# Performance work log

Hardware: AMD Instinct MI355X
Metric: run time of the kernel (lower is better)

Reference implementation:

```python
import jax, jax.numpy as jnp
import numpy as np


def setup_inputs() -> dict:
    key = jax.random.key(0)
    k1, k2, k3, k4, k5 = jax.random.split(key, 5)
    B, S, D, F, E = 4, 4096, 1024, 2048, 8
    top_k = 2
    num_tokens = B * S
    capacity = max(int(num_tokens / E * 1.25), 4)  # 2560
    scale = 0.02
    return {
        "x": jax.random.normal(k1, (B, S, D), dtype=jnp.float32),
        "gate_w": jax.random.normal(k2, (D, E), dtype=jnp.float32) * scale,
        "w_gate": jax.random.normal(k3, (E, D, F), dtype=jnp.float32) * scale,
        "w_up": jax.random.normal(k4, (E, D, F), dtype=jnp.float32) * scale,
        "w_down": jax.random.normal(k5, (E, F, D), dtype=jnp.float32) * scale,
        "num_experts": E,
        "top_k": top_k,
        "capacity": capacity,
    }


AUX_LOSS_WEIGHT = 0.01


def reference(x, gate_w, w_gate, w_up, w_down, num_experts, top_k, capacity):
    B, S, D = x.shape
    N = B * S
    x_flat = x.reshape(N, D)

    # ---- Router ----
    logits = x_flat @ gate_w                      # [N, E]
    probs = jax.nn.softmax(logits, axis=-1)
    weights, indices = jax.lax.top_k(probs, top_k)  # [N, K]
    weights = weights / jnp.sum(weights, axis=-1, keepdims=True)

    # ---- Capacity-based dispatch ----
    indices_flat = indices.reshape(-1)            # [N*K]
    x_rep = jnp.repeat(x_flat, top_k, axis=0)     # [N*K, D]
    expert_mask = jax.nn.one_hot(indices_flat, num_experts, dtype=jnp.int32)  # [N*K, E]
    token_priority = jnp.cumsum(expert_mask, axis=0) * expert_mask
    token_rank = jnp.sum(token_priority, axis=1)  # [N*K], 1-based rank within expert
    valid = (token_rank > 0) & (token_rank <= capacity)
    gather_idx = indices_flat * capacity + (token_rank - 1)  # [N*K]

    total_slots = num_experts * capacity
    # drop-mode scatter: invalid rows are sent out-of-bounds and dropped
    safe_idx = jnp.where(valid, gather_idx, total_slots)
    dispatched = jnp.zeros((total_slots, D), dtype=x.dtype)
    dispatched = dispatched.at[safe_idx].set(x_rep, mode="drop")
    dispatched = dispatched.reshape(num_experts, capacity, D)  # [E, C, D]

    # ---- Fused experts (grouped BMM, SwiGLU) ----
    gate = jnp.einsum("ecd,edf->ecf", dispatched, w_gate)
    up = jnp.einsum("ecd,edf->ecf", dispatched, w_up)
    hidden = jax.nn.silu(gate) * up
    expert_out = jnp.einsum("ecf,efd->ecd", hidden, w_down)
    expert_out_flat = expert_out.reshape(total_slots, D)

    # ---- Combine (row-aligned gather; dropped tokens contribute zero) ----
    gathered = expert_out_flat[jnp.clip(gather_idx, 0, total_slots - 1)]
    combined = jnp.where(valid[:, None], gathered, jnp.zeros((), dtype=x.dtype))
    combined = combined.reshape(N, top_k, D)
    output = jnp.sum(combined * weights[:, :, None], axis=1)  # [N, D]

    # ---- Aux load-balance loss ----
    mask = jax.nn.one_hot(indices, num_experts, dtype=jnp.float32).sum(axis=1)  # [N, E]
    f = mask.sum(axis=0) / (N * top_k + 1e-9)
    P = probs.mean(axis=0)
    aux_loss = num_experts * jnp.sum(f * P) * AUX_LOSS_WEIGHT

    return output.reshape(B, S, D), aux_loss
```

## Files before the change

### kernel.cpp

```cpp
#include <hip/hip_runtime.h>
#include <stdint.h>

#define N_TOK 16384
#define DIM   1024
#define NEXP  8
#define FF    2048
#define CAP   2560
#define NSLOT (NEXP*CAP)

using f32x4  = __attribute__((ext_vector_type(4))) float;
using bf16x8 = __attribute__((ext_vector_type(8))) short;

__device__ __forceinline__ unsigned short f2bf(float f){
  union { float f; unsigned u; } c; c.f = f;
  unsigned u = c.u + 0x7FFFu + ((c.u >> 16) & 1u);
  return (unsigned short)(u >> 16);
}
__device__ __forceinline__ float bf2f(unsigned short h){
  union { unsigned u; float f; } c; c.u = ((unsigned)h) << 16; return c.f;
}

__device__ __forceinline__ void gld16(const unsigned short* g, unsigned short* l){
  __builtin_amdgcn_global_load_lds((__attribute__((address_space(1))) void*)(void*)g,
                                   (__attribute__((address_space(3))) void*)l,
                                   16, 0, 0);
}

#define HBAR __builtin_amdgcn_s_barrier()
#define LG0  asm volatile("s_waitcnt lgkmcnt(0)" ::: "memory")

__global__ __launch_bounds__(256) void k_router(
    const float* __restrict__ x, const float* __restrict__ gate_w,
    int* __restrict__ topidx, float* __restrict__ topw,
    float* __restrict__ wavepart)
{
  __shared__ float gwT[NEXP][DIM];
  int tid = threadIdx.x;
  for (int i = tid; i < DIM*NEXP; i += 256) gwT[i & 7][i >> 3] = gate_w[i];
  __syncthreads();
  int wave = tid >> 6, lane = tid & 63;
  int t = blockIdx.x * 4 + wave;
  const float* xr = x + (size_t)t * DIM;
  double acc[NEXP];
  #pragma unroll
  for (int e = 0; e < NEXP; e++) acc[e] = 0.0;
  for (int j = 0; j < DIM/64; j++){
    double xv = (double)xr[lane + 64*j];
    #pragma unroll
    for (int e = 0; e < NEXP; e++) acc[e] += xv * (double)gwT[e][lane + 64*j];
  }
  #pragma unroll
  for (int off = 32; off >= 1; off >>= 1){
    #pragma unroll
    for (int e = 0; e < NEXP; e++) acc[e] += __shfl_xor(acc[e], off, 64);
  }
  if (lane == 0){
    double m = acc[0];
    #pragma unroll
    for (int e = 1; e < NEXP; e++) m = fmax(m, acc[e]);
    double p[NEXP], Z = 0.0;
    #pragma unroll
    for (int e = 0; e < NEXP; e++){ p[e] = exp(acc[e] - m); Z += p[e]; }
    double invZ = 1.0 / Z;
    #pragma unroll
    for (int e = 0; e < NEXP; e++) p[e] *= invZ;
    float4* wp = (float4*)(wavepart + (size_t)t*NEXP);
    wp[0] = make_float4((float)p[0], (float)p[1], (float)p[2], (float)p[3]);
    wp[1] = make_float4((float)p[4], (float)p[5], (float)p[6], (float)p[7]);
    int i0 = 0; double p0 = p[0];
    #pragma unroll
    for (int e = 1; e < NEXP; e++) if (p[e] > p0){ p0 = p[e]; i0 = e; }
    int i1 = (i0 == 0) ? 1 : 0; double p1 = p[i1];
    #pragma unroll
    for (int e = 0; e < NEXP; e++) if (e != i0 && p[e] > p1){ p1 = p[e]; i1 = e; }
    double s = p0 + p1;
    topidx[t*2+0] = i0; topidx[t*2+1] = i1;
    topw [t*2+0] = (float)(p0/s); topw[t*2+1] = (float)(p1/s);
  }
}

__global__ __launch_bounds__(1024) void k_scan_tcv(
    const int* __restrict__ topidx, const float* __restrict__ wavepart,
    int* __restrict__ slot_token, int* __restrict__ tok_slots,
    float* __restrict__ aux_out,
    const float* __restrict__ wg, const float* __restrict__ wu, const float* __restrict__ wd,
    unsigned short* __restrict__ B1, unsigned short* __restrict__ wdT,
    const float* __restrict__ x, unsigned short* __restrict__ xb)
{
  __shared__ uint8_t smem[32768];
  const int t = threadIdx.x;
  const int bidx = blockIdx.x;

  if (bidx == 0){
    int (*sc)[NEXP] = (int(*)[NEXP])smem;
    const int base_i = t * 32;
    int ids[32];
    #pragma unroll
    for (int j = 0; j < 32; j++) ids[j] = topidx[base_i + j];
    int b[NEXP];
    #pragma unroll
    for (int e = 0; e < NEXP; e++) b[e] = 0;
    #pragma unroll
    for (int j = 0; j < 32; j++){
      #pragma unroll
      for (int e = 0; e < NEXP; e++) if (ids[j] == e) b[e]++;
    }
    #pragma unroll
    for (int e = 0; e < NEXP; e++) sc[t][e] = b[e];
    __syncthreads();
    for (int off = 1; off < 1024; off <<= 1){
      int tmp[NEXP];
      #pragma unroll
      for (int e = 0; e < NEXP; e++) tmp[e] = (t >= off) ? sc[t-off][e] : 0;
      __syncthreads();
      #pragma unroll
      for (int e = 0; e < NEXP; e++) sc[t][e] += tmp[e];
      __syncthreads();
    }
    int myb[NEXP];
    #pragma unroll
    for (int e = 0; e < NEXP; e++) myb[e] = sc[t][e] - b[e];
    int cnt[NEXP];
    #pragma unroll
    for (int e = 0; e < NEXP; e++) cnt[e] = sc[1023][e];
    #pragma unroll
    for (int j = 0; j < 32; j++){
      int slot = -1;
      #pragma unroll
      for (int e = 0; e < NEXP; e++){
        if (ids[j] == e){
          int r = myb[e]; myb[e] = r + 1;
          if (r < CAP){
            slot = e*CAP + r;
            slot_token[slot] = (base_i + j) >> 1;
          }
        }
      }
      tok_slots[base_i + j] = slot;
    }
    for (int idx = t; idx < NSLOT; idx += 1024){
      int e2 = idx / CAP, r2 = idx - e2*CAP;
      if (r2 >= cnt[e2]) slot_token[idx] = -1;
    }
    __syncthreads();
    float pe[NEXP];
    #pragma unroll
    for (int e = 0; e < NEXP; e++) pe[e] = 0.f;
    for (int i = t; i < N_TOK; i += 1024){
      const float4* pr = (const float4*)(wavepart + (size_t)i*NEXP);
      float4 v0 = pr[0], v1 = pr[1];
      pe[0] += v0.x; pe[1] += v0.y; pe[2] += v0.z; pe[3] += v0.w;
      pe[4] += v1.x; pe[5] += v1.y; pe[6] += v1.z; pe[7] += v1.w;
    }
    #pragma unroll
    for (int off = 32; off >= 1; off >>= 1){
      #pragma unroll
      for (int e = 0; e < NEXP; e++) pe[e] += __shfl_xor(pe[e], off, 64);
    }
    __syncthreads();
    float* scf = (float*)smem;
    const int wv = t >> 6, ln = t & 63;
    if (ln == 0){
      #pragma unroll
      for (int e = 0; e < NEXP; e++) scf[wv*NEXP + e] = pe[e];
    }
    __syncthreads();
    if (t == 0){
      float aux = 0.f;
      #pragma unroll
      for (int e = 0; e < NEXP; e++){
        float P = 0.f;
        for (int w = 0; w < 16; w++) P += scf[w*NEXP + e];
        P /= (float)N_TOK;
        float f = (float)cnt[e] / ((float)(N_TOK*2) + 1e-9f);
        aux += f * P;
      }
      aux_out[0] = (float)NEXP * aux * 0.01f;
    }
  } else if (bidx <= 12288){
    float (*tt)[65] = (float(*)[65])smem;
    const int bid = bidx - 1;
    const int z = bid >> 9, rem = bid & 511;
    const int mode = z >> 3, e = z & 7;
    const float* in; unsigned short* out; int R, C, ct, rt;
    if (mode < 2){
      in  = (mode == 0 ? wg : wu) + (size_t)e * DIM * FF;
      out = B1 + (size_t)e * 2 * FF * DIM;
      R = DIM; C = FF; ct = rem & 31; rt = rem >> 5;
    } else {
      in  = wd + (size_t)e * FF * DIM;
      out = wdT + (size_t)e * DIM * FF;
      R = FF; C = DIM; ct = rem >> 5; rt = rem & 31;
    }
    const int c0 = ct * 64, r0 = rt * 64;
    {
      int row = t >> 4, c4 = t & 15;
      float4 v = *(const float4*)(in + (size_t)(r0 + row)*C + c0 + c4*4);
      tt[c4*4+0][row] = v.x; tt[c4*4+1][row] = v.y;
      tt[c4*4+2][row] = v.z; tt[c4*4+3][row] = v.w;
    }
    __syncthreads();
    {
      int cl = t >> 4;
      int rs = (t & 15) * 4;
      int c  = c0 + cl;
      int orow = (mode == 0) ? ((c>>4)*32 + (c&15))
               : (mode == 1) ? ((c>>4)*32 + 16 + (c&15))
               : c;
      unsigned long long pk = 0;
      #pragma unroll
      for (int j = 0; j < 4; j++) pk |= (unsigned long long)f2bf(tt[cl][rs+j]) << (16*j);
      *(unsigned long long*)(out + (size_t)orow*R + r0 + rs) = pk;
    }
  } else {
    const int gb = bidx - 12289;
    size_t base = ((size_t)gb*1024 + t)*4;
    float4 v = *(const float4*)(x + base);
    unsigned long long pk =
        (unsigned long long)f2bf(v.x)
      | ((unsigned long long)f2bf(v.y) << 16)
      | ((unsigned long long)f2bf(v.z) << 32)
      | ((unsigned long long)f2bf(v.w) << 48);
    *(unsigned long long*)(xb + base) = pk;
  }
}

__device__ __forceinline__ void stg(const unsigned short* gsrc, int ldg,
                                    unsigned short* Lh, int wave, int lane){
  const int sl = (lane & 3) ^ ((lane >> 3) & 3);
  #pragma unroll
  for (int j = 0; j < 2; j++){
    int bi = wave*2 + j;
    gld16(gsrc + (size_t)(bi*16 + (lane >> 2))*ldg + sl*8, Lh + bi*512);
  }
}
__device__ __forceinline__ void stgA_ind(const unsigned short* xb, int tok0, int tok1, int k0,
                                         unsigned short* Lh, int wave, int lane){
  const int sl = (lane & 3) ^ ((lane >> 3) & 3);
  gld16(xb + (size_t)tok0*DIM + k0 + sl*8, Lh + (wave*2+0)*512);
  gld16(xb + (size_t)tok1*DIM + k0 + sl*8, Lh + (wave*2+1)*512);
}
__device__ __forceinline__ bf16x8 frd(const unsigned short* Lh, int r, int g){
  return *(const bf16x8*)(Lh + r*32 + (((g ^ ((r >> 1) & 3))) << 3));
}
template<int MG>
__device__ __forceinline__ void mm16(f32x4 (&acc)[8][4], const bf16x8 (&a)[4], const bf16x8 (&b)[4]){
  #pragma unroll
  for (int i = 0; i < 4; i++)
    #pragma unroll
    for (int n = 0; n < 4; n++)
      acc[MG*4+i][n] = __builtin_amdgcn_mfma_f32_16x16x32_bf16(a[i], b[n], acc[MG*4+i][n], 0, 0, 0);
}

#define STG_A(HH, NS)                                                           \
  { if (EPI == 1) stgA_ind(A, tokA0, tokA1, (HH)*32, NS, wave, lane);           \
    else          stg(Ab + (size_t)(HH)*32, LDG, NS, wave, lane); }

#define HALF_STEP(RS, DOSTG, VMW, HH)                                           \
  {                                                                             \
    unsigned short* LA = lds + (RS)*16384;                                      \
    unsigned short* LB = LA + 8192;                                             \
    unsigned short* NS = lds + (((RS)+3)&3)*16384;                              \
    bf16x8 a[4], b[4];                                                          \
    _Pragma("unroll")                                                           \
    for (int i = 0; i < 4; i++) a[i] = frd(LA, wr*128 + i*16 + l15, g);         \
    _Pragma("unroll")                                                           \
    for (int n = 0; n < 4; n++) b[n] = frd(LB, wc*64 + n*16 + l15, g);          \
    if (DOSTG) STG_A(HH, NS);                                                   \
    HBAR; LG0;                                                                  \
    __builtin_amdgcn_s_setprio(1);  mm16<0>(acc, a, b);                         \
    __builtin_amdgcn_s_setprio(0);                                              \
    HBAR;                                                                       \
    _Pragma("unroll")                                                           \
    for (int i = 0; i < 4; i++) a[i] = frd(LA, wr*128 + (4+i)*16 + l15, g);     \
    if (DOSTG) stg(Bb + (size_t)(HH)*32, LDG, NS + 8192, wave, lane);           \
    HBAR; LG0;                                                                  \
    __builtin_amdgcn_s_setprio(1);  mm16<1>(acc, a, b);                         \
    __builtin_amdgcn_s_setprio(0);                                              \
    if ((VMW) == 4) { asm volatile("s_waitcnt vmcnt(4)" ::: "memory"); }        \
    else if ((VMW) == 0) { asm volatile("s_waitcnt vmcnt(0)" ::: "memory"); }   \
    HBAR;                                                                       \
  }

template<int KDIM, int LDG, int EPI>
__global__ __launch_bounds__(512, 2) void k_gemm8(
    const unsigned short* __restrict__ A,
    const unsigned short* __restrict__ B,
    unsigned short* __restrict__ Out0,
    unsigned short* __restrict__ Out1,
    const int* __restrict__ slot_token)
{
  constexpr int NH    = KDIM / 32;
  constexpr int BROWS = (EPI == 1) ? 2*FF : DIM;
  constexpr int LDO   = (EPI == 1) ? FF : DIM;
  __shared__ unsigned short lds[65536];
  const int id = blockIdx.x;
  const int e  = id & 7;
  int t  = id >> 3;
  int ks = 0;
  if (EPI == 2){ ks = t & 1; t >>= 1; }
  const int mt = t % 10, nt = t / 10;
  const int m0 = mt*256, n0 = nt*256;
  const unsigned short* Ab = A + ((size_t)e*CAP   + m0) * LDG + (size_t)ks*KDIM;
  const unsigned short* Bb = B + ((size_t)e*BROWS + n0) * LDG + (size_t)ks*KDIM;
  const int tid = threadIdx.x, wave = tid >> 6, lane = tid & 63;
  const int wr = wave >> 2, wc = wave & 3;
  const int g = lane >> 4, l15 = lane & 15;

  int tokA0 = 0, tokA1 = 0;
  if (EPI == 1){
    int r0 = m0 + (wave*2+0)*16 + (lane >> 2);
    int r1 = m0 + (wave*2+1)*16 + (lane >> 2);
    int t0 = slot_token[e*CAP + r0];
    int t1 = slot_token[e*CAP + r1];
    tokA0 = (t0 < 0) ? 0 : t0;
    tokA1 = (t1 < 0) ? 0 : t1;
  }

  f32x4 acc[8][4];
  const f32x4 z4 = {0.f,0.f,0.f,0.f};
  #pragma unroll
  for (int i = 0; i < 8; i++)
    #pragma unroll
    for (int n = 0; n < 4; n++) acc[i][n] = z4;

  STG_A(0, lds + 0*16384);
  stg(Bb,      LDG, lds + 0*16384 + 8192, wave, lane);
  STG_A(1, lds + 1*16384);
  stg(Bb + 32, LDG, lds + 1*16384 + 8192, wave, lane);
  STG_A(2, lds + 2*16384);
  stg(Bb + 64, LDG, lds + 2*16384 + 8192, wave, lane);
  asm volatile("s_waitcnt vmcnt(4)" ::: "memory");
  HBAR;

  for (int h = 0; h + 8 <= NH; h += 4){
    HALF_STEP(0, true, -1, h+3);
    HALF_STEP(1, true,  4, h+4);
    HALF_STEP(2, true, -1, h+5);
    HALF_STEP(3, true,  4, h+6);
  }
  HALF_STEP(0, true, -1, NH-1);
  HALF_STEP(1, false, 0, 0);
  HALF_STEP(2, false, -1, 0);
  HALF_STEP(3, false, -1, 0);

  if (EPI == 1){
    unsigned short* H = Out0 + ((size_t)e*CAP + m0 + wr*128) * (size_t)LDO;
    const int hc0 = (n0 + wc*64) >> 1;
    #pragma unroll
    for (int mf = 0; mf < 8; mf++)
      #pragma unroll
      for (int q = 0; q < 4; q++){
        int r = mf*16 + g*4 + q;
        #pragma unroll
        for (int p = 0; p < 2; p++){
          float gg = acc[mf][2*p][q], uu = acc[mf][2*p+1][q];
          float h = gg / (1.f + __expf(-gg)) * uu;
          H[(size_t)r*LDO + hc0 + p*16 + l15] = f2bf(h);
        }
      }
  } else {
    unsigned short* P = (ks ? Out1 : Out0);
    unsigned short* O = P + ((size_t)e*CAP + m0 + wr*128) * (size_t)LDO + n0 + wc*64;
    #pragma unroll
    for (int mf = 0; mf < 8; mf++)
      #pragma unroll
      for (int q = 0; q < 4; q++){
        int r = mf*16 + g*4 + q;
        #pragma unroll
        for (int n = 0; n < 4; n++)
          O[(size_t)r*LDO + n*16 + l15] = f2bf(acc[mf][n][q]);
      }
  }
}

__global__ __launch_bounds__(256) void k_combine(
    const unsigned short* __restrict__ P0, const unsigned short* __restrict__ P1,
    const int* __restrict__ tok_slots, const float* __restrict__ topw,
    float* __restrict__ out)
{
  const int t = blockIdx.x*2 + (threadIdx.x >> 7);
  const int tid = threadIdx.x & 127;
  const int s0 = tok_slots[t*2+0], s1 = tok_slots[t*2+1];
  const float w0 = topw[t*2+0], w1 = topw[t*2+1];
  float r[8];
  #pragma unroll
  for (int j = 0; j < 8; j++) r[j] = 0.f;
  if (s0 >= 0){
    bf16x8 v0 = *(const bf16x8*)(P0 + (size_t)s0*DIM + tid*8);
    bf16x8 v1 = *(const bf16x8*)(P1 + (size_t)s0*DIM + tid*8);
    #pragma unroll
    for (int j = 0; j < 8; j++)
      r[j] += w0 * (bf2f((unsigned short)v0[j]) + bf2f((unsigned short)v1[j]));
  }
  if (s1 >= 0){
    bf16x8 v0 = *(const bf16x8*)(P0 + (size_t)s1*DIM + tid*8);
    bf16x8 v1 = *(const bf16x8*)(P1 + (size_t)s1*DIM + tid*8);
    #pragma unroll
    for (int j = 0; j < 8; j++)
      r[j] += w1 * (bf2f((unsigned short)v0[j]) + bf2f((unsigned short)v1[j]));
  }
  float4* o = (float4*)(out + (size_t)t*DIM + tid*8);
  o[0] = make_float4(r[0], r[1], r[2], r[3]);
  o[1] = make_float4(r[4], r[5], r[6], r[7]);
}

extern "C" void kernel_launch(void* const* d_in, const int* in_sizes, int n_in,
                              void* d_out, int out_size, void* d_ws, size_t ws_size,
                              hipStream_t stream)
{
  const float* x      = (const float*)d_in[0];
  const float* gate_w = (const float*)d_in[1];
  const float* w_gate = (const float*)d_in[2];
  const float* w_up   = (const float*)d_in[3];
  const float* w_down = (const float*)d_in[4];
  float* out = (float*)d_out;

  uint8_t* ws = (uint8_t*)d_ws;
  int*   topidx       = (int*)ws;               ws += (size_t)N_TOK*2*4;
  float* topw         = (float*)ws;             ws += (size_t)N_TOK*2*4;
  int*   slot_token   = (int*)ws;               ws += (size_t)NSLOT*4;
  int*   tok_slots    = (int*)ws;               ws += (size_t)N_TOK*2*4;
  float* wavepart     = (float*)ws;             ws += (size_t)N_TOK*NEXP*4;
  unsigned short* xb     = (unsigned short*)ws; ws += (size_t)N_TOK*DIM*2;
  unsigned short* P0     = (unsigned short*)ws; ws += (size_t)NSLOT*DIM*2;
  unsigned short* hidden = (unsigned short*)ws; ws += (size_t)NSLOT*FF*2;
  unsigned short* B1     = (unsigned short*)ws; ws += (size_t)NEXP*2*FF*DIM*2;
  unsigned short* wdT    = (unsigned short*)ws; ws += (size_t)NEXP*DIM*FF*2;
  size_t need = (size_t)(ws - (uint8_t*)d_ws);
  if (ws_size < need) return;
  unsigned short* P1 = B1;

  k_router<<<N_TOK/4, 256, 0, stream>>>(x, gate_w, topidx, topw, wavepart);
  k_scan_tcv<<<16385, 1024, 0, stream>>>(topidx, wavepart, slot_token, tok_slots,
                                         out + (size_t)N_TOK*DIM,
                                         w_gate, w_up, w_down, B1, wdT, x, xb);
  k_gemm8<DIM, DIM, 1><<<1280, 512, 0, stream>>>(xb, B1, hidden, nullptr, slot_token);
  k_gemm8<DIM, FF, 2><<<640, 512, 0, stream>>>(hidden, wdT, P0, P1, nullptr);
  k_combine<<<N_TOK/2, 256, 0, stream>>>(P0, P1, tok_slots, topw, out);
}
```

Baseline: 435.9 us.

## Restructure expert GEMM mainloop to 64-wide K tiles with double-buffered quarter staging

The GEMM main loop changes from four-stage 32-wide K half-steps to a two-buffer scheme with 64-wide K tiles. Each buffer is split into A and B halves that are staged separately and interleaved with four MFMA quadrant groups. The LDS swizzle is now 8-slot XOR, and token row offsets are precomputed per lane. The goal is fewer barriers per K element and better overlap of global-to-LDS loads with MFMA, at the cost of more register-held fragments and a more fragile wait-count schedule.

```diff
diff --git a/kernel.cpp b/kernel.cpp
--- a/kernel.cpp
+++ b/kernel.cpp
@@ -225,62 +225,32 @@
   }
 }
 
-__device__ __forceinline__ void stg(const unsigned short* gsrc, int ldg,
-                                    unsigned short* Lh, int wave, int lane){
-  const int sl = (lane & 3) ^ ((lane >> 3) & 3);
-  #pragma unroll
-  for (int j = 0; j < 2; j++){
-    int bi = wave*2 + j;
-    gld16(gsrc + (size_t)(bi*16 + (lane >> 2))*ldg + sl*8, Lh + bi*512);
-  }
-}
-__device__ __forceinline__ void stgA_ind(const unsigned short* xb, int tok0, int tok1, int k0,
-                                         unsigned short* Lh, int wave, int lane){
-  const int sl = (lane & 3) ^ ((lane >> 3) & 3);
-  gld16(xb + (size_t)tok0*DIM + k0 + sl*8, Lh + (wave*2+0)*512);
-  gld16(xb + (size_t)tok1*DIM + k0 + sl*8, Lh + (wave*2+1)*512);
-}
-__device__ __forceinline__ bf16x8 frd(const unsigned short* Lh, int r, int g){
-  return *(const bf16x8*)(Lh + r*32 + (((g ^ ((r >> 1) & 3))) << 3));
-}
-template<int MG>
-__device__ __forceinline__ void mm16(f32x4 (&acc)[8][4], const bf16x8 (&a)[4], const bf16x8 (&b)[4]){
-  #pragma unroll
-  for (int i = 0; i < 4; i++)
-    #pragma unroll
-    for (int n = 0; n < 4; n++)
-      acc[MG*4+i][n] = __builtin_amdgcn_mfma_f32_16x16x32_bf16(a[i], b[n], acc[MG*4+i][n], 0, 0, 0);
-}
-
-#define STG_A(HH, NS)                                                           \
-  { if (EPI == 1) stgA_ind(A, tokA0, tokA1, (HH)*32, NS, wave, lane);           \
-    else          stg(Ab + (size_t)(HH)*32, LDG, NS, wave, lane); }
-
-#define HALF_STEP(RS, DOSTG, VMW, HH)                                           \
-  {                                                                             \
-    unsigned short* LA = lds + (RS)*16384;                                      \
-    unsigned short* LB = LA + 8192;                                             \
-    unsigned short* NS = lds + (((RS)+3)&3)*16384;                              \
-    bf16x8 a[4], b[4];                                                          \
-    _Pragma("unroll")                                                           \
-    for (int i = 0; i < 4; i++) a[i] = frd(LA, wr*128 + i*16 + l15, g);         \
-    _Pragma("unroll")                                                           \
-    for (int n = 0; n < 4; n++) b[n] = frd(LB, wc*64 + n*16 + l15, g);          \
-    if (DOSTG) STG_A(HH, NS);                                                   \
-    HBAR; LG0;                                                                  \
-    __builtin_amdgcn_s_setprio(1);  mm16<0>(acc, a, b);                         \
-    __builtin_amdgcn_s_setprio(0);                                              \
-    HBAR;                                                                       \
-    _Pragma("unroll")                                                           \
-    for (int i = 0; i < 4; i++) a[i] = frd(LA, wr*128 + (4+i)*16 + l15, g);     \
-    if (DOSTG) stg(Bb + (size_t)(HH)*32, LDG, NS + 8192, wave, lane);           \
-    HBAR; LG0;                                                                  \
-    __builtin_amdgcn_s_setprio(1);  mm16<1>(acc, a, b);                         \
-    __builtin_amdgcn_s_setprio(0);                                              \
-    if ((VMW) == 4) { asm volatile("s_waitcnt vmcnt(4)" ::: "memory"); }        \
-    else if ((VMW) == 0) { asm volatile("s_waitcnt vmcnt(0)" ::: "memory"); }   \
-    HBAR;                                                                       \
-  }
+#define FRD(R_, RR, KS) (*(const bf16x8*)((R_) + (RR)*64 + ((((KS)) ^ l7) << 3)))
+
+#define STGH(TYPE, KT2) {                                                          \
+    unsigned short* R_ = lds + ((((KT2)&1)*4 + (TYPE)))*8192;                      \
+    if ((TYPE) < 2){                                                               \
+      if (EPI == 1){                                                               \
+        gld16(Axb + aoff[(TYPE)&1][0] + (KT2)*64, R_ + (wave*8)*64);               \
+        gld16(Axb + aoff[(TYPE)&1][1] + (KT2)*64, R_ + (64 + wave*8)*64);          \
+      } else {                                                                     \
+        gld16(a00 + (size_t)(((TYPE)&1)*128 +  0)*LDG + (KT2)*64, R_ + (wave*8)*64);      \
+        gld16(a00 + (size_t)(((TYPE)&1)*128 + 64)*LDG + (KT2)*64, R_ + (64 + wave*8)*64); \
+      }                                                                            \
+    } else {                                                                       \
+      gld16(b00 + (size_t)(((TYPE)&1)*128 +  0)*LDG + (KT2)*64, R_ + (wave*8)*64);        \
+      gld16(b00 + (size_t)(((TYPE)&1)*128 + 64)*LDG + (KT2)*64, R_ + (64 + wave*8)*64);   \
+    } }
+
+#define MM8(AM, AN, AV, BV)                                                        \
+  _Pragma("unroll")                                                                \
+  for (int f = 0; f < 4; f++)                                                      \
+    _Pragma("unroll")                                                              \
+    for (int n = 0; n < 2; n++)                                                    \
+      _Pragma("unroll")                                                            \
+      for (int kk = 0; kk < 2; kk++)                                               \
+        acc[(AM)+f][(AN)+n] = __builtin_amdgcn_mfma_f32_16x16x32_bf16(             \
+            AV[f*2+kk], BV[n*2+kk], acc[(AM)+f][(AN)+n], 0, 0, 0);
 
 template<int KDIM, int LDG, int EPI>
 __global__ __launch_bounds__(512, 2) void k_gemm8(
@@ -290,7 +260,7 @@
     unsigned short* __restrict__ Out1,
     const int* __restrict__ slot_token)
 {
-  constexpr int NH    = KDIM / 32;
+  constexpr int NT    = KDIM / 64;
   constexpr int BROWS = (EPI == 1) ? 2*FF : DIM;
   constexpr int LDO   = (EPI == 1) ? FF : DIM;
   __shared__ unsigned short lds[65536];
@@ -305,16 +275,23 @@
   const unsigned short* Bb = B + ((size_t)e*BROWS + n0) * LDG + (size_t)ks*KDIM;
   const int tid = threadIdx.x, wave = tid >> 6, lane = tid & 63;
   const int wr = wave >> 2, wc = wave & 3;
-  const int g = lane >> 4, l15 = lane & 15;
-
-  int tokA0 = 0, tokA1 = 0;
+  const int g = lane >> 4, l15 = lane & 15, l7 = l15 & 7;
+  const int srow = lane >> 3, sslot = lane & 7;
+  const int kslot_src = sslot ^ srow;
+
+  const unsigned short* Axb = A + (size_t)kslot_src*8;
+  unsigned int aoff[2][2];
+  const unsigned short* a00 = Ab + (size_t)(wave*8 + srow)*LDG + kslot_src*8;
+  const unsigned short* b00 = Bb + (size_t)(wave*8 + srow)*LDG + kslot_src*8;
   if (EPI == 1){
-    int r0 = m0 + (wave*2+0)*16 + (lane >> 2);
-    int r1 = m0 + (wave*2+1)*16 + (lane >> 2);
-    int t0 = slot_token[e*CAP + r0];
-    int t1 = slot_token[e*CAP + r1];
-    tokA0 = (t0 < 0) ? 0 : t0;
-    tokA1 = (t1 < 0) ? 0 : t1;
+    #pragma unroll
+    for (int ah = 0; ah < 2; ah++)
+      #pragma unroll
+      for (int j = 0; j < 2; j++){
+        int row = m0 + ah*128 + j*64 + wave*8 + srow;
+        int tk = slot_token[e*CAP + row];
+        aoff[ah][j] = (unsigned)((tk < 0 ? 0 : tk) * DIM);
+      }
   }
 
   f32x4 acc[8][4];
@@ -324,25 +301,56 @@
     #pragma unroll
     for (int n = 0; n < 4; n++) acc[i][n] = z4;
 
-  STG_A(0, lds + 0*16384);
-  stg(Bb,      LDG, lds + 0*16384 + 8192, wave, lane);
-  STG_A(1, lds + 1*16384);
-  stg(Bb + 32, LDG, lds + 1*16384 + 8192, wave, lane);
-  STG_A(2, lds + 2*16384);
-  stg(Bb + 64, LDG, lds + 2*16384 + 8192, wave, lane);
-  asm volatile("s_waitcnt vmcnt(4)" ::: "memory");
+  STGH(0,0); STGH(1,0); STGH(2,0); STGH(3,0);
+  STGH(0,1); STGH(1,1); STGH(2,1);
+  asm volatile("s_waitcnt vmcnt(6)" ::: "memory");
   HBAR;
 
-  for (int h = 0; h + 8 <= NH; h += 4){
-    HALF_STEP(0, true, -1, h+3);
-    HALF_STEP(1, true,  4, h+4);
-    HALF_STEP(2, true, -1, h+5);
-    HALF_STEP(3, true,  4, h+6);
-  }
-  HALF_STEP(0, true, -1, NH-1);
-  HALF_STEP(1, false, 0, 0);
-  HALF_STEP(2, false, -1, 0);
-  HALF_STEP(3, false, -1, 0);
+  for (int kt = 0; kt < NT; ++kt){
+    const int b0 = (kt & 1)*4;
+    unsigned short* RA = lds + (b0 + wr)*8192;
+    unsigned short* RB = lds + (b0 + 2 + (wc >> 1))*8192;
+    const int nb = (wc & 1)*64;
+    bf16x8 a0[8], a1[8], bv[4], b2[4];
+
+    #pragma unroll
+    for (int f = 0; f < 4; f++)
+      #pragma unroll
+      for (int kk = 0; kk < 2; kk++)
+        a0[f*2+kk] = FRD(RA, f*16 + l15, kk*4 + g);
+    #pragma unroll
+    for (int n = 0; n < 2; n++)
+      #pragma unroll
+      for (int kk = 0; kk < 2; kk++)
+        bv[n*2+kk] = FRD(RB, nb + n*16 + l15, kk*4 + g);
+    if (kt + 1 < NT) STGH(3, kt+1);
+    HBAR; LG0;
+    __builtin_amdgcn_s_setprio(1);  MM8(0, 0, a0, bv);  __builtin_amdgcn_s_setprio(0);
+
+    #pragma unroll
+    for (int f = 0; f < 4; f++)
+      #pragma unroll
+      for (int kk = 0; kk < 2; kk++)
+        a1[f*2+kk] = FRD(RA, 64 + f*16 + l15, kk*4 + g);
+    if (kt + 2 < NT) STGH(0, kt+2);
+    HBAR; LG0;
+    __builtin_amdgcn_s_setprio(1);  MM8(4, 0, a1, bv);  __builtin_amdgcn_s_setprio(0);
+
+    #pragma unroll
+    for (int n = 0; n < 2; n++)
+      #pragma unroll
+      for (int kk = 0; kk < 2; kk++)
+        b2[n*2+kk] = FRD(RB, nb + 32 + n*16 + l15, kk*4 + g);
+    if (kt + 2 < NT) STGH(1, kt+2);
+    HBAR; LG0;
+    __builtin_amdgcn_s_setprio(1);  MM8(4, 2, a1, b2);  __builtin_amdgcn_s_setprio(0);
+
+    if (kt + 2 < NT) STGH(2, kt+2);
+    __builtin_amdgcn_s_setprio(1);  MM8(0, 2, a0, b2);  __builtin_amdgcn_s_setprio(0);
+    if (kt <= NT-3)      { asm volatile("s_waitcnt vmcnt(6)" ::: "memory"); }
+    else if (kt == NT-2) { asm volatile("s_waitcnt vmcnt(0)" ::: "memory"); }
+    HBAR;
+  }
 
   if (EPI == 1){
     unsigned short* H = Out0 + ((size_t)e*CAP + m0 + wr*128) * (size_t)LDO;
```

New measurement: 423.3 us (median of 3 runs). 1.03x faster.
